# Optimization experiments

Hardware: AMD Instinct MI355X
Metric: run time of the kernel (lower is better)

The kernel has to match this reference:

```python
import jax, jax.numpy as jnp
import numpy as np

B, F, D_IN, H, OUT = 32768, 200, 5, 15, 30

def setup_inputs() -> dict:
    key = jax.random.key(0)
    ks = jax.random.split(key, 7)
    return {
        "y":  jax.random.normal(ks[0], (B, F, D_IN), dtype=jnp.float32),
        "W1": jax.random.normal(ks[1], (F, D_IN, H), dtype=jnp.float32) * 0.3,
        "b1": jax.random.normal(ks[2], (F, H), dtype=jnp.float32) * 0.1,
        "W2": jax.random.normal(ks[3], (F, H, OUT), dtype=jnp.float32) * 0.2,
        "b2": jax.random.normal(ks[4], (F, OUT), dtype=jnp.float32) * 0.1,
        "W3": jax.random.normal(ks[5], (F * OUT, 1), dtype=jnp.float32) * 0.02,
        "b3": jax.random.normal(ks[6], (1,), dtype=jnp.float32) * 0.1,
    }

def reference(y, W1, b1, W2, b2, W3, b3):
    # 200 independent tiny 2-layer MLPs, batched over the feature axis f.
    # Note: original applies ReLU only AFTER the second Linear.
    h1 = jnp.einsum('bfi,fih->bfh', y, W1) + b1          # [B, F, H]
    h2 = jax.nn.relu(jnp.einsum('bfh,fho->bfo', h1, W2) + b2)  # [B, F, OUT]
    flat = h2.reshape(h2.shape[0], -1)                   # concat along feature axis -> [B, F*OUT]
    return flat @ W3 + b3                                # [B, 1]
```

## Files before the change

### kernel.cpp

```cpp
#include <hip/hip_runtime.h>

#define B_TOTAL 32768
#define NF 200
#define D_IN 5
#define NH 15
#define NOUT 30
#define RECS 216

typedef float v2f __attribute__((ext_vector_type(2)));
typedef float v4f __attribute__((ext_vector_type(4)));

__global__ __launch_bounds__(256) void precompute_kernel(
    const float* __restrict__ W1, const float* __restrict__ b1,
    const float* __restrict__ W2, const float* __restrict__ b2,
    const float* __restrict__ W3, float* __restrict__ rec)
{
    const int f = blockIdx.x;
    const int t = threadIdx.x;
    float* r = rec + f * RECS;
    if (t < NOUT) {
        const int o = t;
        float s = b2[f * NOUT + o];
        #pragma unroll
        for (int h = 0; h < NH; ++h)
            s = fmaf(b1[f * NH + h], W2[(f * NH + h) * NOUT + o], s);
        r[o] = s;
    } else if (t < 2 * NOUT) {
        const int o = t - NOUT;
        r[NOUT + o] = W3[f * NOUT + o];
    } else if (t < 2 * NOUT + D_IN * NOUT) {
        const int j = t - 2 * NOUT;
        const int i = j / NOUT;
        const int o = j - i * NOUT;
        float s = 0.f;
        #pragma unroll
        for (int h = 0; h < NH; ++h)
            s = fmaf(W1[(f * D_IN + i) * NH + h], W2[(f * NH + h) * NOUT + o], s);
        r[2 * NOUT + i * NOUT + o] = s;
    }
}

#define BTILE 64
#define NSUB 10
#define FSUB 20
#define NCHUNK 5

__global__ __launch_bounds__(640, 5) void mlp_kernel(
    const float* __restrict__ y, const float* __restrict__ rec,
    const float* __restrict__ b3, float* __restrict__ out)
{
    __shared__ float red[BTILE * NSUB];

    const int tid   = threadIdx.x;
    const int lane  = tid & 63;
    const int sub   = tid >> 6;
    const int sub_u = __builtin_amdgcn_readfirstlane(sub);
    const int b0    = blockIdx.x * BTILE;
    const int b     = b0 + lane;

    const v4f* __restrict__ yq =
        (const v4f*)(y + (size_t)b * (NF * D_IN) + sub_u * (FSUB * D_IN));
    const float* __restrict__ wrec = rec + (size_t)sub_u * FSUB * RECS;

    v2f acc0 = (v2f)0.0f, acc1 = (v2f)0.0f;

    #pragma unroll 1
    for (int cc = 0; cc < NCHUNK; ++cc) {
        v4f yv[5];
        #pragma unroll
        for (int j = 0; j < 5; ++j) yv[j] = yq[cc * 5 + j];

        #pragma unroll
        for (int k = 0; k < 4; ++k) {
            const float* __restrict__ r  = wrec + (cc * 4 + k) * RECS;
            const v2f* __restrict__ rb   = (const v2f*)r;
            const v2f* __restrict__ rw3  = (const v2f*)(r + NOUT);
            const v2f* __restrict__ rw   = (const v2f*)(r + 2 * NOUT);

            v2f z[15];
            {
                const int e = k * 5;
                const float y0 = yv[e >> 2][e & 3];
                #pragma unroll
                for (int p = 0; p < 15; ++p) z[p] = rb[p] + y0 * rw[p];
            }
            #pragma unroll
            for (int i = 1; i < D_IN; ++i) {
                const int e = k * 5 + i;
                const float yi = yv[e >> 2][e & 3];
                #pragma unroll
                for (int p = 0; p < 15; ++p) z[p] += yi * rw[i * 15 + p];
            }
            #pragma unroll
            for (int p = 0; p < 15; ++p) {
                v2f zr = __builtin_elementwise_max(z[p], (v2f)0.0f);
                if (p & 1) acc1 += zr * rw3[p];
                else       acc0 += zr * rw3[p];
            }
        }
    }

    v2f accs = acc0 + acc1;
    red[lane * NSUB + sub] = accs.x + accs.y;
    __syncthreads();

    if (tid < BTILE) {
        float s = b3[0];
        #pragma unroll
        for (int k = 0; k < NSUB; ++k) s += red[tid * NSUB + k];
        out[b0 + tid] = s;
    }
}

extern "C" void kernel_launch(void* const* d_in, const int* in_sizes, int n_in,
                              void* d_out, int out_size, void* d_ws, size_t ws_size,
                              hipStream_t stream) {
    const float* y  = (const float*)d_in[0];
    const float* W1 = (const float*)d_in[1];
    const float* b1 = (const float*)d_in[2];
    const float* W2 = (const float*)d_in[3];
    const float* b2 = (const float*)d_in[4];
    const float* W3 = (const float*)d_in[5];
    const float* b3 = (const float*)d_in[6];
    float* out = (float*)d_out;

    float* rec = (float*)d_ws;

    precompute_kernel<<<NF, 256, 0, stream>>>(W1, b1, W2, b2, W3, rec);
    mlp_kernel<<<B_TOTAL / BTILE, BTILE * NSUB, 0, stream>>>(y, rec, b3, out);
}
```

Measured before the change: 229.4 us.

## Split features across grid, stage folded weights in LDS, reduce with shuffles and atomics

Reworks the main kernel so each block handles 64 batch rows and 40 features. The folded per-feature weights are packed into an interleaved 16-lane output-pair layout and staged in shared memory. Each lane computes two outputs for four batch rows, and partial sums are combined with 16-wide shuffles, then atomically added to an output buffer zeroed by a memset. The aim is fewer scalar and global weight loads per FMA and more parallelism across the grid. The cost is redundant y loads across the 16 lanes of a group, an extra memset launch, and atomic adds.

```diff
diff --git a/kernel.cpp b/kernel.cpp
--- a/kernel.cpp
+++ b/kernel.cpp
@@ -5,7 +5,8 @@
 #define D_IN 5
 #define NH 15
 #define NOUT 30
-#define RECS 216
+#define NOP 16
+
 
 typedef float v2f __attribute__((ext_vector_type(2)));
 typedef float v4f __attribute__((ext_vector_type(4)));
@@ -13,102 +14,145 @@
 __global__ __launch_bounds__(256) void precompute_kernel(
     const float* __restrict__ W1, const float* __restrict__ b1,
     const float* __restrict__ W2, const float* __restrict__ b2,
-    const float* __restrict__ W3, float* __restrict__ rec)
+    const float* __restrict__ W3, float* __restrict__ rec2)
 {
-    const int f = blockIdx.x;
-    const int t = threadIdx.x;
-    float* r = rec + f * RECS;
-    if (t < NOUT) {
-        const int o = t;
+    const int idx = blockIdx.x * 256 + threadIdx.x;
+    if (idx >= NF * NOP) return;
+    const int f  = idx / NOP;
+    const int op = idx - f * NOP;
+    float* r = rec2 + (size_t)f * 256;
+
+    if (op == 15) {
+        #pragma unroll
+        for (int j = 0; j < 4; ++j) {
+            r[j * 64 + op * 4 + 0] = 0.f; r[j * 64 + op * 4 + 1] = 0.f;
+            r[j * 64 + op * 4 + 2] = 0.f; r[j * 64 + op * 4 + 3] = 0.f;
+        }
+        return;
+    }
+    const int o0 = 2 * op, o1 = 2 * op + 1;
+
+    float bcv[2], wc[D_IN][2];
+    #pragma unroll
+    for (int t = 0; t < 2; ++t) {
+        const int o = (t == 0) ? o0 : o1;
         float s = b2[f * NOUT + o];
         #pragma unroll
         for (int h = 0; h < NH; ++h)
             s = fmaf(b1[f * NH + h], W2[(f * NH + h) * NOUT + o], s);
-        r[o] = s;
-    } else if (t < 2 * NOUT) {
-        const int o = t - NOUT;
-        r[NOUT + o] = W3[f * NOUT + o];
-    } else if (t < 2 * NOUT + D_IN * NOUT) {
-        const int j = t - 2 * NOUT;
-        const int i = j / NOUT;
-        const int o = j - i * NOUT;
-        float s = 0.f;
+        bcv[t] = s;
         #pragma unroll
-        for (int h = 0; h < NH; ++h)
-            s = fmaf(W1[(f * D_IN + i) * NH + h], W2[(f * NH + h) * NOUT + o], s);
-        r[2 * NOUT + i * NOUT + o] = s;
+        for (int i = 0; i < D_IN; ++i) {
+            float w = 0.f;
+            #pragma unroll
+            for (int h = 0; h < NH; ++h)
+                w = fmaf(W1[(f * D_IN + i) * NH + h], W2[(f * NH + h) * NOUT + o], w);
+            wc[i][t] = w;
+        }
     }
+    r[0 * 64 + op * 4 + 0] = bcv[0];
+    r[0 * 64 + op * 4 + 1] = bcv[1];
+    r[0 * 64 + op * 4 + 2] = W3[f * NOUT + o0];
+    r[0 * 64 + op * 4 + 3] = W3[f * NOUT + o1];
+    r[1 * 64 + op * 4 + 0] = wc[0][0];
+    r[1 * 64 + op * 4 + 1] = wc[0][1];
+    r[1 * 64 + op * 4 + 2] = wc[1][0];
+    r[1 * 64 + op * 4 + 3] = wc[1][1];
+    r[2 * 64 + op * 4 + 0] = wc[2][0];
+    r[2 * 64 + op * 4 + 1] = wc[2][1];
+    r[2 * 64 + op * 4 + 2] = wc[3][0];
+    r[2 * 64 + op * 4 + 3] = wc[3][1];
+    r[3 * 64 + op * 4 + 0] = wc[4][0];
+    r[3 * 64 + op * 4 + 1] = wc[4][1];
+    r[3 * 64 + op * 4 + 2] = 0.f;
+    r[3 * 64 + op * 4 + 3] = 0.f;
 }
 
-#define BTILE 64
-#define NSUB 10
-#define FSUB 20
-#define NCHUNK 5
+#define FPART 40
+#define NPARTS 5
 
-__global__ __launch_bounds__(640, 5) void mlp_kernel(
-    const float* __restrict__ y, const float* __restrict__ rec,
+__global__ __launch_bounds__(256, 3) void mlp_kernel(
+    const float* __restrict__ y, const float* __restrict__ rec2,
     const float* __restrict__ b3, float* __restrict__ out)
 {
-    __shared__ float red[BTILE * NSUB];
+    __shared__ v4f shw[FPART * 4 * NOP];
 
-    const int tid   = threadIdx.x;
-    const int lane  = tid & 63;
-    const int sub   = tid >> 6;
-    const int sub_u = __builtin_amdgcn_readfirstlane(sub);
-    const int b0    = blockIdx.x * BTILE;
-    const int b     = b0 + lane;
+    const int tid = threadIdx.x;
+    const int f0  = blockIdx.y * FPART;
 
-    const v4f* __restrict__ yq =
-        (const v4f*)(y + (size_t)b * (NF * D_IN) + sub_u * (FSUB * D_IN));
-    const float* __restrict__ wrec = rec + (size_t)sub_u * FSUB * RECS;
+    {
+        const v4f* gsrc = (const v4f*)(rec2 + (size_t)f0 * 256);
+        #pragma unroll
+        for (int i = 0; i < 10; ++i)
+            shw[tid + i * 256] = gsrc[tid + i * 256];
+    }
 
-    v2f acc0 = (v2f)0.0f, acc1 = (v2f)0.0f;
+    const int l   = tid & 63;
+    const int wv  = tid >> 6;
+    const int bsu = l >> 4;
+    const int op  = l & 15;
+    const int bb  = blockIdx.x * 64 + wv * 16 + bsu * 4;
+
+    const v4f* yr[4];
+    #pragma unroll
+    for (int bl = 0; bl < 4; ++bl)
+        yr[bl] = (const v4f*)(y + (size_t)(bb + bl) * (NF * D_IN) + f0 * D_IN);
+
+    v2f acc[4] = {(v2f)0.f, (v2f)0.f, (v2f)0.f, (v2f)0.f};
+
+    __syncthreads();
 
     #pragma unroll 1
-    for (int cc = 0; cc < NCHUNK; ++cc) {
-        v4f yv[5];
+    for (int g = 0; g < FPART / 4; ++g) {
+        v4f yv[4][5];
         #pragma unroll
-        for (int j = 0; j < 5; ++j) yv[j] = yq[cc * 5 + j];
+        for (int bl = 0; bl < 4; ++bl)
+            #pragma unroll
+            for (int j = 0; j < 5; ++j)
+                yv[bl][j] = yr[bl][g * 5 + j];
 
         #pragma unroll
         for (int k = 0; k < 4; ++k) {
-            const float* __restrict__ r  = wrec + (cc * 4 + k) * RECS;
-            const v2f* __restrict__ rb   = (const v2f*)r;
-            const v2f* __restrict__ rw3  = (const v2f*)(r + NOUT);
-            const v2f* __restrict__ rw   = (const v2f*)(r + 2 * NOUT);
+            const int fl = g * 4 + k;
+            const v4f w0  = shw[(fl * 4 + 0) * NOP + op];
+            const v4f w1  = shw[(fl * 4 + 1) * NOP + op];
+            const v4f w2  = shw[(fl * 4 + 2) * NOP + op];
+            const v4f w3q = shw[(fl * 4 + 3) * NOP + op];
 
-            v2f z[15];
-            {
-                const int e = k * 5;
-                const float y0 = yv[e >> 2][e & 3];
-                #pragma unroll
-                for (int p = 0; p < 15; ++p) z[p] = rb[p] + y0 * rw[p];
-            }
             #pragma unroll
-            for (int i = 1; i < D_IN; ++i) {
-                const int e = k * 5 + i;
-                const float yi = yv[e >> 2][e & 3];
-                #pragma unroll
-                for (int p = 0; p < 15; ++p) z[p] += yi * rw[i * 15 + p];
-            }
-            #pragma unroll
-            for (int p = 0; p < 15; ++p) {
-                v2f zr = __builtin_elementwise_max(z[p], (v2f)0.0f);
-                if (p & 1) acc1 += zr * rw3[p];
-                else       acc0 += zr * rw3[p];
+            for (int bl = 0; bl < 4; ++bl) {
+                const float yb0 = yv[bl][(k * 5 + 0) >> 2][(k * 5 + 0) & 3];
+                const float yb1 = yv[bl][(k * 5 + 1) >> 2][(k * 5 + 1) & 3];
+                const float yb2 = yv[bl][(k * 5 + 2) >> 2][(k * 5 + 2) & 3];
+                const float yb3 = yv[bl][(k * 5 + 3) >> 2][(k * 5 + 3) & 3];
+                const float yb4 = yv[bl][(k * 5 + 4) >> 2][(k * 5 + 4) & 3];
+
+                v2f z = (v2f){w0.x, w0.y} + yb0 * (v2f){w1.x, w1.y};
+                z += yb1 * (v2f){w1.z, w1.w};
+                z += yb2 * (v2f){w2.x, w2.y};
+                z += yb3 * (v2f){w2.z, w2.w};
+                z += yb4 * (v2f){w3q.x, w3q.y};
+                z  = __builtin_elementwise_max(z, (v2f)0.0f);
+                acc[bl] += z * (v2f){w0.z, w0.w};
             }
         }
     }
 
-    v2f accs = acc0 + acc1;
-    red[lane * NSUB + sub] = accs.x + accs.y;
-    __syncthreads();
-
-    if (tid < BTILE) {
-        float s = b3[0];
-        #pragma unroll
-        for (int k = 0; k < NSUB; ++k) s += red[tid * NSUB + k];
-        out[b0 + tid] = s;
+    float s0 = acc[0].x + acc[0].y;
+    float s1 = acc[1].x + acc[1].y;
+    float s2 = acc[2].x + acc[2].y;
+    float s3 = acc[3].x + acc[3].y;
+    #pragma unroll
+    for (int m = 1; m < 16; m <<= 1) {
+        s0 += __shfl_xor(s0, m, 16);
+        s1 += __shfl_xor(s1, m, 16);
+        s2 += __shfl_xor(s2, m, 16);
+        s3 += __shfl_xor(s3, m, 16);
+    }
+    if (op < 4) {
+        float v = (op == 0) ? s0 : (op == 1) ? s1 : (op == 2) ? s2 : s3;
+        if (blockIdx.y == 0) v += b3[0];
+        atomicAdd(&out[bb + op], v);
     }
 }
 
@@ -124,8 +168,9 @@
     const float* b3 = (const float*)d_in[6];
     float* out = (float*)d_out;
 
-    float* rec = (float*)d_ws;
+    float* rec2 = (float*)d_ws;
 
-    precompute_kernel<<<NF, 256, 0, stream>>>(W1, b1, W2, b2, W3, rec);
-    mlp_kernel<<<B_TOTAL / BTILE, BTILE * NSUB, 0, stream>>>(y, rec, b3, out);
+    hipMemsetAsync(out, 0, (size_t)B_TOTAL * sizeof(float), stream);
+    precompute_kernel<<<(NF * NOP + 255) / 256, 256, 0, stream>>>(W1, b1, W2, b2, W3, rec2);
+    mlp_kernel<<<dim3(B_TOTAL / 64, NPARTS), 256, 0, stream>>>(y, rec2, b3, out);
 }
```

Measured after the change: 270.7 us. +18.0%, slower.
